# Kernel tuning notes

Hardware: AMD Instinct MI355X
Metric: run time of the kernel (lower is better)

The kernel has to match this reference:

```python
import jax, jax.numpy as jnp
import numpy as np

N, E = 50000, 800000
IN_DIM, OUT_DIM, HEADS, ORDER = 128, 32, 4, 2
HID = OUT_DIM * HEADS  # 128
NEG_SLOPE = 0.2
LN_EPS = 1e-5


def setup_inputs() -> dict:
    key = jax.random.key(0)
    ks = jax.random.split(key, 16)
    inp = {
        'features': jax.random.normal(ks[0], (N, IN_DIM), jnp.float32),
        'src': jax.random.randint(ks[1], (E,), 0, N, jnp.int32),
        'dst': jax.random.randint(ks[2], (E,), 0, N, jnp.int32),
    }
    in_dims = [IN_DIM, HID]
    for i in range(ORDER):
        d_in = in_dims[i]
        s = 1.0 / np.sqrt(d_in)
        inp[f'W{i}'] = jax.random.normal(ks[3 + 5 * i], (d_in, HID), jnp.float32) * s
        inp[f'al{i}'] = jax.random.normal(ks[4 + 5 * i], (HEADS, OUT_DIM), jnp.float32) * 0.1
        inp[f'ar{i}'] = jax.random.normal(ks[5 + 5 * i], (HEADS, OUT_DIM), jnp.float32) * 0.1
        inp[f'b{i}'] = jnp.zeros((HID,), jnp.float32)
        inp[f'g{i}'] = jnp.ones((HID,), jnp.float32)
        inp[f'be{i}'] = jnp.zeros((HID,), jnp.float32)
    return inp


def _gat_layer(x, src, dst, W, al, ar, b):
    # x: [N, d_in] -> h: [N, H, D]
    h = (x @ W).reshape(N, HEADS, OUT_DIM)
    el = jnp.sum(h * al, axis=-1)  # [N, H]
    er = jnp.sum(h * ar, axis=-1)  # [N, H]
    e = jax.nn.leaky_relu(el[src] + er[dst], NEG_SLOPE)  # [E, H]
    # segment softmax over incoming edges of each dst node
    m = jax.ops.segment_max(e, dst, num_segments=N)  # [N, H]
    ex = jnp.exp(e - m[dst])  # [E, H]
    denom = jax.ops.segment_sum(ex, dst, num_segments=N)  # [N, H]
    alpha = ex / jnp.maximum(denom[dst], 1e-9)  # [E, H]
    msg = h[src] * alpha[:, :, None]  # [E, H, D]
    out = jax.ops.segment_sum(msg, dst, num_segments=N)  # [N, H, D]
    return out.reshape(N, HID) + b


def _layernorm(x, g, be):
    mu = jnp.mean(x, axis=-1, keepdims=True)
    var = jnp.mean(jnp.square(x - mu), axis=-1, keepdims=True)
    return (x - mu) * jax.lax.rsqrt(var + LN_EPS) * g + be


def reference(features, src, dst, W0, al0, ar0, b0, g0, be0, W1, al1, ar1, b1, g1, be1):
    feats = features
    params = [(W0, al0, ar0, b0, g0, be0), (W1, al1, ar1, b1, g1, be1)]
    for (W, al, ar, b, g, be) in params:
        feats = _gat_layer(feats, src, dst, W, al, ar, b)
        feats = _layernorm(feats, g, be)
        feats = jax.nn.elu(feats)
    return feats
```

## Files before the change

kernel.cpp:

```cpp
#include <hip/hip_runtime.h>
#include <hip/hip_bf16.h>

#define N_NODES 50000
#define E_EDGES 800000
#define HID 128
#define HEADS 4
#define NEG_SLOPE 0.2f
#define LN_EPS 1e-5f
#define PARAM_FLOATS 17024
#define NBUCK 196
#define BCAP 6144
#define BIN_CH 2048
#define CVT_BLOCKS 67

typedef __attribute__((ext_vector_type(8))) short short8;
typedef __attribute__((ext_vector_type(4))) float float4v;
typedef __fp16 hf2 __attribute__((ext_vector_type(2)));

__device__ __forceinline__ float bf2f(__hip_bfloat16 b) { return __bfloat162float(b); }
__device__ __forceinline__ short bfb(float f) {
    __hip_bfloat16 h = __float2bfloat16(f);
    return *(short*)&h;
}
__device__ __forceinline__ float leaky(float v) { return v > 0.f ? v : v * NEG_SLOPE; }

__device__ __forceinline__ unsigned int f2ord(float f) {
    unsigned int u = __float_as_uint(f);
    return (u & 0x80000000u) ? ~u : (u | 0x80000000u);
}
__device__ __forceinline__ float ord2f(unsigned int u) {
    u = (u & 0x80000000u) ? (u & 0x7FFFFFFFu) : ~u;
    return __uint_as_float(u);
}

__device__ __forceinline__ unsigned int pair_lo(unsigned int a, unsigned int b) {
#if __has_builtin(__builtin_amdgcn_perm)
    return __builtin_amdgcn_perm(b, a, 0x05040100);
#else
    return (a & 0xFFFFu) | (b << 16);
#endif
}
__device__ __forceinline__ unsigned int pair_hi(unsigned int a, unsigned int b) {
#if __has_builtin(__builtin_amdgcn_perm)
    return __builtin_amdgcn_perm(b, a, 0x07060302);
#else
    return (a >> 16) | (b & 0xFFFF0000u);
#endif
}
__device__ __forceinline__ float dot2acc(unsigned int hpair, unsigned int epair, float acc) {
#if __has_builtin(__builtin_amdgcn_fdot2)
    return __builtin_amdgcn_fdot2(__builtin_bit_cast(hf2, hpair),
                                  __builtin_bit_cast(hf2, epair), acc, false);
#else
    hf2 hv = __builtin_bit_cast(hf2, hpair);
    hf2 ev = __builtin_bit_cast(hf2, epair);
    return fmaf((float)hv.x, (float)ev.x, fmaf((float)hv.y, (float)ev.y, acc));
#endif
}
__device__ __forceinline__ unsigned int pk_f16x2(float a, float b) {
#if __has_builtin(__builtin_amdgcn_cvt_pkrtz)
    auto r = __builtin_amdgcn_cvt_pkrtz(a, b);
    return __builtin_bit_cast(unsigned int, r);
#else
    hf2 r = { (__fp16)a, (__fp16)b };
    return __builtin_bit_cast(unsigned int, r);
#endif
}

__global__ __launch_bounds__(256) void cvt_params_kernel(
    const void* W0, const void* al0, const void* ar0, const void* b0,
    const void* g0, const void* be0,
    const void* W1, const void* al1, const void* ar1, const void* b1,
    const void* g1, const void* be1,
    float* __restrict__ out0, float* __restrict__ out1,
    unsigned short* __restrict__ wt0, unsigned short* __restrict__ wt1,
    unsigned int* __restrict__ flag, unsigned int* __restrict__ gmax0,
    unsigned int* __restrict__ gmax1, int* __restrict__ bcnt) {
    int t = threadIdx.x;
    const unsigned int* w0p = (const unsigned int*)W0;
    int cnt = 0;
    for (int i = t; i < 4096; i += 256) {
        unsigned int lo = (w0p[i] & 0xFFFFu) << 16;
        float v = fabsf(__uint_as_float(lo));
        if (v >= 1e-6f && v <= 1.0f) cnt++;
    }
#pragma unroll
    for (int off = 32; off >= 1; off >>= 1) cnt += __shfl_xor(cnt, off);
    __shared__ int shm[4];
    if ((t & 63) == 0) shm[t >> 6] = cnt;
    __syncthreads();
    unsigned int isb = ((shm[0] + shm[1] + shm[2] + shm[3]) > 2048) ? 1u : 0u;

    if (blockIdx.x == 0) {
        if (t == 0) *flag = isb;
        if (t < 4) {
            gmax0[t] = f2ord(-INFINITY);
            gmax1[t] = f2ord(-INFINITY);
        }
        if (t < NBUCK) bcnt[t] = 0;
    }

    int blk = blockIdx.x;
    int layer = 0;
    if (blk >= CVT_BLOCKS) { layer = 1; blk -= CVT_BLOCKS; }
    int i = blk * 256 + t;
    if (i >= PARAM_FLOATS) return;

    const void *W, *al, *ar, *b, *g, *be;
    float* out;
    unsigned short* wt;
    if (layer == 0) {
        W = W0; al = al0; ar = ar0; b = b0; g = g0; be = be0;
        out = out0; wt = wt0;
    } else {
        W = W1; al = al1; ar = ar1; b = b1; g = g1; be = be1;
        out = out1; wt = wt1;
    }

    if (i < 16384) {
        unsigned short bits;
        if (isb) bits = ((const unsigned short*)W)[i];
        else     { short s = bfb(((const float*)W)[i]); bits = (unsigned short)s; }
        wt[((i & 127) << 7) | (i >> 7)] = bits;
        return;
    }
    const void* src; int off;
    if (i < 16512)      { src = al; off = i - 16384; }
    else if (i < 16640) { src = ar; off = i - 16512; }
    else if (i < 16768) { src = b;  off = i - 16640; }
    else if (i < 16896) { src = g;  off = i - 16768; }
    else                { src = be; off = i - 16896; }
    out[i] = isb ? bf2f(((const __hip_bfloat16*)src)[off]) : ((const float*)src)[off];
}

__global__ __launch_bounds__(256) void bin_kernel(const int* __restrict__ src,
                                                  const int* __restrict__ dst,
                                                  int* __restrict__ bcnt,
                                                  unsigned int* __restrict__ ebuf) {
    __shared__ int lh[NBUCK];
    __shared__ int lbase[NBUCK];
    int t = threadIdx.x;
    for (int i = t; i < NBUCK; i += 256) lh[i] = 0;
    __syncthreads();
    int e0 = blockIdx.x * BIN_CH;
    int n = min(BIN_CH, E_EDGES - e0);
    int s8[8], d8[8], rk[8];
#pragma unroll
    for (int j = 0; j < 8; ++j) {
        int k = j * 256 + t;
        if (k < n) {
            s8[j] = src[e0 + k];
            d8[j] = dst[e0 + k];
            rk[j] = atomicAdd(&lh[d8[j] >> 8], 1);
        }
    }
    __syncthreads();
    for (int i = t; i < NBUCK; i += 256) lbase[i] = atomicAdd(&bcnt[i], lh[i]);
    __syncthreads();
#pragma unroll
    for (int j = 0; j < 8; ++j) {
        int k = j * 256 + t;
        if (k < n) {
            int b = d8[j] >> 8;
            int pos = lbase[b] + rk[j];
            if (pos < BCAP)
                ebuf[b * BCAP + pos] = ((unsigned int)s8[j] << 8) | (unsigned int)(d8[j] & 255);
        }
    }
}

__global__ __launch_bounds__(256) void csr_kernel(const int* __restrict__ bcnt,
                                                  const unsigned int* __restrict__ ebuf,
                                                  int* __restrict__ offs,
                                                  int* __restrict__ esrc) {
    __shared__ int cnt[256];
    __shared__ int wt[4];
    __shared__ int sbase[256];
    __shared__ int out_lds[BCAP];
    int b = blockIdx.x, t = threadIdx.x;
    int lane = t & 63, wid = t >> 6;

    int bv = (t < NBUCK) ? min(bcnt[t], BCAP) : 0;
    {
        int x = bv;
#pragma unroll
        for (int o = 1; o < 64; o <<= 1) {
            int y = __shfl_up(x, o);
            if (lane >= o) x += y;
        }
        if (lane == 63) wt[wid] = x;
        __syncthreads();
        int add = 0;
        for (int j = 0; j < wid; j++) add += wt[j];
        sbase[t] = add + x - bv;
    }
    __syncthreads();
    int base = sbase[b];
    int n = min(bcnt[b], BCAP);
    const unsigned int* eb = ebuf + b * BCAP;
    cnt[t] = 0;
    __syncthreads();
    for (int i = t; i < n; i += 256) atomicAdd(&cnt[eb[i] & 255u], 1);
    __syncthreads();
    int v = cnt[t];
    int x = v;
#pragma unroll
    for (int o = 1; o < 64; o <<= 1) {
        int y = __shfl_up(x, o);
        if (lane >= o) x += y;
    }
    if (lane == 63) wt[wid] = x;
    __syncthreads();
    int add = 0;
    for (int j = 0; j < wid; j++) add += wt[j];
    int excl = add + x - v;
    int node = b * 256 + t;
    if (node <= N_NODES) offs[node] = base + excl;
    __syncthreads();
    cnt[t] = excl;
    __syncthreads();
    for (int i = t; i < n; i += 256) {
        unsigned int e = eb[i];
        int p = atomicAdd(&cnt[e & 255u], 1);
        out_lds[p] = (int)(e >> 8);
    }
    __syncthreads();
    for (int i = t; i < n; i += 256) esrc[base + i] = out_lds[i];
}

__global__ __launch_bounds__(256) void gemm_mfma_kernel(const void* __restrict__ xin,
                                                        const unsigned short* __restrict__ wt,
                                                        const float* __restrict__ params,
                                                        const unsigned int* __restrict__ flag,
                                                        int mode,
                                                        unsigned int* __restrict__ hh,
                                                        float* __restrict__ el,
                                                        float* __restrict__ er,
                                                        unsigned int* __restrict__ gmax,
                                                        int M) {
    __shared__ float ldsC[4][16][132];
    __shared__ unsigned int smax[4];
    unsigned int isb = mode ? 1u : *flag;
    int t = threadIdx.x;
    if (t < 4) smax[t] = 0u;
    int w = t >> 6, lane = t & 63;
    int m = lane & 15, quad = lane >> 4;
    int row0b = blockIdx.x * 64;
    int arow = row0b + w * 16 + m;
    bool avalid = arow < M;

    float4v acc[8];
#pragma unroll
    for (int i = 0; i < 8; i++) acc[i] = (float4v){0.f, 0.f, 0.f, 0.f};

#pragma unroll
    for (int kt = 0; kt < 4; ++kt) {
        short8 a = (short8){0, 0, 0, 0, 0, 0, 0, 0};
        if (avalid) {
            int base = arow * 128 + kt * 32 + quad * 8;
            if (isb) {
                a = *(const short8*)((const unsigned short*)xin + base);
            } else {
                const float* xp = (const float*)xin + base;
                float4 f0 = *(const float4*)xp;
                float4 f1 = *(const float4*)(xp + 4);
                a = (short8){bfb(f0.x), bfb(f0.y), bfb(f0.z), bfb(f0.w),
                             bfb(f1.x), bfb(f1.y), bfb(f1.z), bfb(f1.w)};
            }
        }
#pragma unroll
        for (int ct = 0; ct < 8; ++ct) {
            short8 b = *(const short8*)(wt + (ct * 16 + m) * 128 + kt * 32 + quad * 8);
            acc[ct] = __builtin_amdgcn_mfma_f32_16x16x32_bf16(a, b, acc[ct], 0, 0, 0);
        }
    }

#pragma unroll
    for (int ct = 0; ct < 8; ++ct)
#pragma unroll
        for (int r = 0; r < 4; ++r)
            ldsC[w][quad * 4 + r][ct * 16 + m] = acc[ct][r];
    __syncthreads();

    int c0 = (t & 15) * 8;
    int r0e = (t >> 4) * 4;
    float al8[8], ar8[8];
#pragma unroll
    for (int j = 0; j < 8; j++) {
        al8[j] = params[16384 + c0 + j];
        ar8[j] = params[16512 + c0 + j];
    }
    int head = (lane & 15) >> 2;
    float elmax = -INFINITY;

#pragma unroll
    for (int i = 0; i < 4; i++) {
        int rr = r0e + i;
        int row = row0b + rr;
        bool ok = row < M;
        const float* ld = &ldsC[rr >> 4][rr & 15][c0];
        float4 h0 = *(const float4*)ld;
        float4 h1 = *(const float4*)(ld + 4);
        float hv[8] = {h0.x, h0.y, h0.z, h0.w, h1.x, h1.y, h1.z, h1.w};
        if (ok) {
            unsigned int u0 = pk_f16x2(hv[0], hv[1]);
            unsigned int u1 = pk_f16x2(hv[2], hv[3]);
            unsigned int u2 = pk_f16x2(hv[4], hv[5]);
            unsigned int u3 = pk_f16x2(hv[6], hv[7]);
            *(uint4*)(hh + row * 64 + (c0 >> 1)) = make_uint4(u0, u1, u2, u3);
        }
        float e_l = 0.f, e_r = 0.f;
#pragma unroll
        for (int j = 0; j < 8; j++) {
            e_l = fmaf(hv[j], al8[j], e_l);
            e_r = fmaf(hv[j], ar8[j], e_r);
        }
        e_l += __shfl_xor(e_l, 1); e_l += __shfl_xor(e_l, 2);
        e_r += __shfl_xor(e_r, 1); e_r += __shfl_xor(e_r, 2);
        if (ok && (lane & 3) == 0) {
            el[row * 4 + head] = e_l;
            er[row * 4 + head] = e_r;
            elmax = fmaxf(elmax, e_l);
        }
    }
    elmax = fmaxf(elmax, __shfl_xor(elmax, 16));
    elmax = fmaxf(elmax, __shfl_xor(elmax, 32));
    __syncthreads();
    if ((lane & 15) == 0 || (lane & 15) == 4 || (lane & 15) == 8 || (lane & 15) == 12) {
        if (elmax > -INFINITY) atomicMax(&smax[head], f2ord(elmax));
    }
    __syncthreads();
    if (t < 4) atomicMax(&gmax[t], smax[t]);
}

template <bool LAST>
__global__ __launch_bounds__(256) void agg_ln_kernel(const int* __restrict__ offs,
                                                     const int* __restrict__ esrc,
                                                     const float* __restrict__ el,
                                                     const float* __restrict__ er,
                                                     const unsigned int* __restrict__ hh,
                                                     const float* __restrict__ params,
                                                     const unsigned int* __restrict__ gmax,
                                                     const unsigned int* __restrict__ flag,
                                                     unsigned int* __restrict__ x_next,
                                                     void* __restrict__ out) {
    int node = (blockIdx.x * 256 + threadIdx.x) >> 6;
    int lane = threadIdx.x & 63;
    if (node >= N_NODES) return;
    int e0 = offs[node], e1 = offs[node + 1];
    int d = e1 - e0;
    int sh = lane & 3;
    int slot = lane >> 2;
    int q = lane >> 4;
    int l4 = lane & 15;
    int hd = l4 >> 2;
    float er_s = er[node * 4 + sh];
    float M = leaky(ord2f(gmax[sh]) + er_s);

    float lsum = 0.f;
    float a0 = 0.f, a1 = 0.f, a2 = 0.f, a3 = 0.f;
    float a4 = 0.f, a5 = 0.f, a6 = 0.f, a7 = 0.f;
    for (int b0 = 0; b0 < d; b0 += 16) {
        int idx = b0 + slot;
        float ex = 0.f;
        int s = 0;
        if (idx < d) {
            s = esrc[e0 + idx];
            ex = __expf(leaky(el[s * 4 + sh] + er_s) - M);
        }
        lsum += ex;
        __fp16 e16 = (__fp16)ex;
        unsigned int pk = ((unsigned int)s << 16)
                        | (unsigned int)__builtin_bit_cast(unsigned short, e16);
#pragma unroll
        for (int jp = 0; jp < 2; ++jp) {
            unsigned int q1 = __shfl(pk, (jp * 8 + q) * 4 + hd);
            unsigned int q2 = __shfl(pk, (jp * 8 + 4 + q) * 4 + hd);
            int s1 = (int)(q1 >> 16);
            int s2 = (int)(q2 >> 16);
            uint4 p = *(const uint4*)(hh + s1 * 64 + l4 * 4);
            uint4 r = *(const uint4*)(hh + s2 * 64 + l4 * 4);
            unsigned int e2 = pair_lo(q1, q2);
            a0 = dot2acc(pair_lo(p.x, r.x), e2, a0);
            a1 = dot2acc(pair_hi(p.x, r.x), e2, a1);
            a2 = dot2acc(pair_lo(p.y, r.y), e2, a2);
            a3 = dot2acc(pair_hi(p.y, r.y), e2, a3);
            a4 = dot2acc(pair_lo(p.z, r.z), e2, a4);
            a5 = dot2acc(pair_hi(p.z, r.z), e2, a5);
            a6 = dot2acc(pair_lo(p.w, r.w), e2, a6);
            a7 = dot2acc(pair_hi(p.w, r.w), e2, a7);
        }
    }
#pragma unroll
    for (int off = 4; off <= 32; off <<= 1) lsum += __shfl_xor(lsum, off);
    float l = __shfl(lsum, hd);
    a0 += __shfl_xor(a0, 16); a0 += __shfl_xor(a0, 32);
    a1 += __shfl_xor(a1, 16); a1 += __shfl_xor(a1, 32);
    a2 += __shfl_xor(a2, 16); a2 += __shfl_xor(a2, 32);
    a3 += __shfl_xor(a3, 16); a3 += __shfl_xor(a3, 32);
    a4 += __shfl_xor(a4, 16); a4 += __shfl_xor(a4, 32);
    a5 += __shfl_xor(a5, 16); a5 += __shfl_xor(a5, 32);
    a6 += __shfl_xor(a6, 16); a6 += __shfl_xor(a6, 32);
    a7 += __shfl_xor(a7, 16); a7 += __shfl_xor(a7, 32);

    float inv = 1.f / fmaxf(l, 1e-9f);
    int c0 = l4 * 8;
    float4 ba = *(const float4*)(params + 16640 + c0);
    float4 bb = *(const float4*)(params + 16640 + c0 + 4);
    float v0 = fmaf(a0, inv, ba.x);
    float v1 = fmaf(a1, inv, ba.y);
    float v2 = fmaf(a2, inv, ba.z);
    float v3 = fmaf(a3, inv, ba.w);
    float v4 = fmaf(a4, inv, bb.x);
    float v5 = fmaf(a5, inv, bb.y);
    float v6 = fmaf(a6, inv, bb.z);
    float v7 = fmaf(a7, inv, bb.w);

    float s1 = (v0 + v1) + (v2 + v3) + (v4 + v5) + (v6 + v7);
    float s2 = (v0 * v0 + v1 * v1) + (v2 * v2 + v3 * v3)
             + (v4 * v4 + v5 * v5) + (v6 * v6 + v7 * v7);
#pragma unroll
    for (int off = 1; off <= 8; off <<= 1) {
        s1 += __shfl_xor(s1, off);
        s2 += __shfl_xor(s2, off);
    }
    float mu = s1 * (1.f / 128.f);
    float var = fmaxf(s2 * (1.f / 128.f) - mu * mu, 0.f);
    float rstd = rsqrtf(var + LN_EPS);
    float4 ga = *(const float4*)(params + 16768 + c0);
    float4 gb = *(const float4*)(params + 16768 + c0 + 4);
    float4 ea = *(const float4*)(params + 16896 + c0);
    float4 eb = *(const float4*)(params + 16896 + c0 + 4);
    float y0 = (v0 - mu) * rstd * ga.x + ea.x;
    float y1 = (v1 - mu) * rstd * ga.y + ea.y;
    float y2 = (v2 - mu) * rstd * ga.z + ea.z;
    float y3 = (v3 - mu) * rstd * ga.w + ea.w;
    float y4 = (v4 - mu) * rstd * gb.x + eb.x;
    float y5 = (v5 - mu) * rstd * gb.y + eb.y;
    float y6 = (v6 - mu) * rstd * gb.z + eb.z;
    float y7 = (v7 - mu) * rstd * gb.w + eb.w;
    y0 = y0 > 0.f ? y0 : (__expf(y0) - 1.f);
    y1 = y1 > 0.f ? y1 : (__expf(y1) - 1.f);
    y2 = y2 > 0.f ? y2 : (__expf(y2) - 1.f);
    y3 = y3 > 0.f ? y3 : (__expf(y3) - 1.f);
    y4 = y4 > 0.f ? y4 : (__expf(y4) - 1.f);
    y5 = y5 > 0.f ? y5 : (__expf(y5) - 1.f);
    y6 = y6 > 0.f ? y6 : (__expf(y6) - 1.f);
    y7 = y7 > 0.f ? y7 : (__expf(y7) - 1.f);

    if (q == 0) {
        if (LAST && !*flag) {
            *(float4*)((float*)out + node * 128 + c0) = make_float4(y0, y1, y2, y3);
            *(float4*)((float*)out + node * 128 + c0 + 4) = make_float4(y4, y5, y6, y7);
        } else {
            uint4 pk4;
            pk4.x = (unsigned int)(unsigned short)bfb(y0)
                  | ((unsigned int)(unsigned short)bfb(y1) << 16);
            pk4.y = (unsigned int)(unsigned short)bfb(y2)
                  | ((unsigned int)(unsigned short)bfb(y3) << 16);
            pk4.z = (unsigned int)(unsigned short)bfb(y4)
                  | ((unsigned int)(unsigned short)bfb(y5) << 16);
            pk4.w = (unsigned int)(unsigned short)bfb(y6)
                  | ((unsigned int)(unsigned short)bfb(y7) << 16);
            unsigned int* dst = LAST ? (unsigned int*)out : x_next;
            *(uint4*)(dst + node * 64 + l4 * 4) = pk4;
        }
    }
}

extern "C" void kernel_launch(void* const* d_in, const int* in_sizes, int n_in,
                              void* d_out, int out_size, void* d_ws, size_t ws_size,
                              hipStream_t stream) {
    const void* features = d_in[0];
    const int* src = (const int*)d_in[1];
    const int* dst = (const int*)d_in[2];

    char* w = (char*)d_ws;
    unsigned int* xbuf = (unsigned int*)w;
    unsigned int* hh = (unsigned int*)(w + 12800000);
    float* el = (float*)(w + 25600000);
    float* er = (float*)(w + 26400000);
    float* params0 = (float*)(w + 27200000);
    float* params1 = params0 + PARAM_FLOATS;
    unsigned short* wt0 = (unsigned short*)(w + 27337000);
    unsigned short* wt1 = wt0 + 16384;
    int* offs = (int*)(w + 27403000);
    int* esrc = (int*)(w + 27604000);
    int* bcnt  = (int*)(w + 30804992);
    unsigned int* flag  = (unsigned int*)(w + 30806848);
    unsigned int* gmax0 = (unsigned int*)(w + 30806912);
    unsigned int* gmax1 = (unsigned int*)(w + 30806976);
    unsigned int* ebuf = (unsigned int*)(w + 30807040);

    cvt_params_kernel<<<2 * CVT_BLOCKS, 256, 0, stream>>>(
        d_in[3], d_in[4], d_in[5], d_in[6], d_in[7], d_in[8],
        d_in[9], d_in[10], d_in[11], d_in[12], d_in[13], d_in[14],
        params0, params1, wt0, wt1, flag, gmax0, gmax1, bcnt);

    bin_kernel<<<(E_EDGES + BIN_CH - 1) / BIN_CH, 256, 0, stream>>>(src, dst, bcnt, ebuf);
    csr_kernel<<<NBUCK, 256, 0, stream>>>(bcnt, ebuf, offs, esrc);

    for (int l = 0; l < 2; ++l) {
        float* params = (l == 0) ? params0 : params1;
        unsigned short* wt = (l == 0) ? wt0 : wt1;
        unsigned int* gmax = (l == 0) ? gmax0 : gmax1;
        const void* x = (l == 0) ? features : (const void*)xbuf;
        int mode = (l == 0) ? 0 : 1;

        gemm_mfma_kernel<<<(N_NODES + 63) / 64, 256, 0, stream>>>(
            x, wt, params, flag, mode, hh, el, er, gmax, N_NODES);
        if (l == 0) {
            agg_ln_kernel<false><<<(N_NODES * 64 + 255) / 256, 256, 0, stream>>>(
                offs, esrc, el, er, hh, params, gmax, flag, xbuf, nullptr);
        } else {
            agg_ln_kernel<true><<<(N_NODES * 64 + 255) / 256, 256, 0, stream>>>(
                offs, esrc, el, er, hh, params, gmax, flag, nullptr, d_out);
        }
    }
}
```

Before: 259.3 us.

## Precompute per-edge exp weights in separate kernel, simplify aggregation loop

Adds an edge-parallel kernel that computes the four per-head softmax numerators for every CSR edge and packs them with the source index into a 16-byte record. The aggregation kernel then reads these records directly instead of gathering el/er, computing exp, and shuffling packed values between lanes. The per-head denominator is accumulated with a dot2 against ones. The CSR stage now also stores the destination node alongside the source. This removes the shuffles and the redundant exp work from the latency-bound gather loop, at the cost of an extra launch per layer and about 12.8 MB of extra writes and reads per layer. The denominator is now summed from fp16-rounded values.

```diff
diff --git a/kernel.cpp b/kernel.cpp
--- a/kernel.cpp
+++ b/kernel.cpp
@@ -33,6 +33,14 @@
     return __uint_as_float(u);
 }
 
+__device__ __forceinline__ unsigned int pair_sel(unsigned int a, unsigned int b,
+                                                 unsigned int pmask, int hi) {
+#if __has_builtin(__builtin_amdgcn_perm)
+    return __builtin_amdgcn_perm(b, a, pmask);
+#else
+    return hi ? ((a >> 16) | (b & 0xFFFF0000u)) : ((a & 0xFFFFu) | (b << 16));
+#endif
+}
 __device__ __forceinline__ unsigned int pair_lo(unsigned int a, unsigned int b) {
 #if __has_builtin(__builtin_amdgcn_perm)
     return __builtin_amdgcn_perm(b, a, 0x05040100);
@@ -172,7 +180,7 @@
 __global__ __launch_bounds__(256) void csr_kernel(const int* __restrict__ bcnt,
                                                   const unsigned int* __restrict__ ebuf,
                                                   int* __restrict__ offs,
-                                                  int* __restrict__ esrc) {
+                                                  unsigned int* __restrict__ edat) {
     __shared__ int cnt[256];
     __shared__ int wt[4];
     __shared__ int sbase[256];
@@ -222,10 +230,13 @@
     for (int i = t; i < n; i += 256) {
         unsigned int e = eb[i];
         int p = atomicAdd(&cnt[e & 255u], 1);
-        out_lds[p] = (int)(e >> 8);
-    }
-    __syncthreads();
-    for (int i = t; i < n; i += 256) esrc[base + i] = out_lds[i];
+        out_lds[p] = (int)e;
+    }
+    __syncthreads();
+    for (int i = t; i < n; i += 256) {
+        unsigned int e = (unsigned int)out_lds[i];
+        edat[base + i] = ((e >> 8) << 16) | ((unsigned int)(b * 256) + (e & 255u));
+    }
 }
 
 __global__ __launch_bounds__(256) void gemm_mfma_kernel(const void* __restrict__ xin,
@@ -333,14 +344,38 @@
     if (t < 4) atomicMax(&gmax[t], smax[t]);
 }
 
+__global__ __launch_bounds__(256) void edge_ex_kernel(const unsigned int* __restrict__ edat,
+                                                      const float* __restrict__ el,
+                                                      const float* __restrict__ er,
+                                                      const unsigned int* __restrict__ gmax,
+                                                      uint4* __restrict__ exb) {
+    int p = blockIdx.x * 256 + threadIdx.x;
+    if (p >= E_EDGES) {
+        if (p < E_EDGES + 16) exb[p] = make_uint4(0, 0, 0, 0);
+        return;
+    }
+    unsigned int u = edat[p];
+    int s = (int)(u >> 16);
+    int dn = (int)(u & 0xFFFFu);
+    float4 elv = *(const float4*)(el + s * 4);
+    float4 erv = *(const float4*)(er + dn * 4);
+    float elvv[4] = {elv.x, elv.y, elv.z, elv.w};
+    float ervv[4] = {erv.x, erv.y, erv.z, erv.w};
+    float ex[4];
+#pragma unroll
+    for (int h = 0; h < 4; ++h) {
+        float M = leaky(ord2f(gmax[h]) + ervv[h]);
+        float e = leaky(elvv[h] + ervv[h]);
+        ex[h] = __expf(e - M);
+    }
+    exb[p] = make_uint4((unsigned int)s, pk_f16x2(ex[0], ex[1]), pk_f16x2(ex[2], ex[3]), 0u);
+}
+
 template <bool LAST>
 __global__ __launch_bounds__(256) void agg_ln_kernel(const int* __restrict__ offs,
-                                                     const int* __restrict__ esrc,
-                                                     const float* __restrict__ el,
-                                                     const float* __restrict__ er,
+                                                     const uint4* __restrict__ exb,
                                                      const unsigned int* __restrict__ hh,
                                                      const float* __restrict__ params,
-                                                     const unsigned int* __restrict__ gmax,
                                                      const unsigned int* __restrict__ flag,
                                                      unsigned int* __restrict__ x_next,
                                                      void* __restrict__ out) {
@@ -349,51 +384,42 @@
     if (node >= N_NODES) return;
     int e0 = offs[node], e1 = offs[node + 1];
     int d = e1 - e0;
-    int sh = lane & 3;
-    int slot = lane >> 2;
     int q = lane >> 4;
     int l4 = lane & 15;
     int hd = l4 >> 2;
-    float er_s = er[node * 4 + sh];
-    float M = leaky(ord2f(gmax[sh]) + er_s);
+    unsigned int pmask = (hd & 1) ? 0x07060302u : 0x05040100u;
+    int wsel_hi = (hd & 2) >> 1;
+    const unsigned int ONEPAIR = 0x3C003C00u;
+    const uint4* exbp = exb + e0;
 
     float lsum = 0.f;
     float a0 = 0.f, a1 = 0.f, a2 = 0.f, a3 = 0.f;
     float a4 = 0.f, a5 = 0.f, a6 = 0.f, a7 = 0.f;
     for (int b0 = 0; b0 < d; b0 += 16) {
-        int idx = b0 + slot;
-        float ex = 0.f;
-        int s = 0;
-        if (idx < d) {
-            s = esrc[e0 + idx];
-            ex = __expf(leaky(el[s * 4 + sh] + er_s) - M);
-        }
-        lsum += ex;
-        __fp16 e16 = (__fp16)ex;
-        unsigned int pk = ((unsigned int)s << 16)
-                        | (unsigned int)__builtin_bit_cast(unsigned short, e16);
 #pragma unroll
         for (int jp = 0; jp < 2; ++jp) {
-            unsigned int q1 = __shfl(pk, (jp * 8 + q) * 4 + hd);
-            unsigned int q2 = __shfl(pk, (jp * 8 + 4 + q) * 4 + hd);
-            int s1 = (int)(q1 >> 16);
-            int s2 = (int)(q2 >> 16);
-            uint4 p = *(const uint4*)(hh + s1 * 64 + l4 * 4);
-            uint4 r = *(const uint4*)(hh + s2 * 64 + l4 * 4);
-            unsigned int e2 = pair_lo(q1, q2);
-            a0 = dot2acc(pair_lo(p.x, r.x), e2, a0);
-            a1 = dot2acc(pair_hi(p.x, r.x), e2, a1);
-            a2 = dot2acc(pair_lo(p.y, r.y), e2, a2);
-            a3 = dot2acc(pair_hi(p.y, r.y), e2, a3);
-            a4 = dot2acc(pair_lo(p.z, r.z), e2, a4);
-            a5 = dot2acc(pair_hi(p.z, r.z), e2, a5);
-            a6 = dot2acc(pair_lo(p.w, r.w), e2, a6);
-            a7 = dot2acc(pair_hi(p.w, r.w), e2, a7);
-        }
-    }
-#pragma unroll
-    for (int off = 4; off <= 32; off <<= 1) lsum += __shfl_xor(lsum, off);
-    float l = __shfl(lsum, hd);
+            int ia = b0 + jp * 8 + q;
+            int ib = ia + 4;
+            uint4 eqA = (ia < d) ? exbp[ia] : make_uint4(0, 0, 0, 0);
+            uint4 eqB = (ib < d) ? exbp[ib] : make_uint4(0, 0, 0, 0);
+            int sA = (int)eqA.x, sB = (int)eqB.x;
+            unsigned int wA = wsel_hi ? eqA.z : eqA.y;
+            unsigned int wB = wsel_hi ? eqB.z : eqB.y;
+            unsigned int epair = pair_sel(wA, wB, pmask, hd & 1);
+            uint4 p = *(const uint4*)(hh + sA * 64 + l4 * 4);
+            uint4 r = *(const uint4*)(hh + sB * 64 + l4 * 4);
+            lsum = dot2acc(epair, ONEPAIR, lsum);
+            a0 = dot2acc(pair_lo(p.x, r.x), epair, a0);
+            a1 = dot2acc(pair_hi(p.x, r.x), epair, a1);
+            a2 = dot2acc(pair_lo(p.y, r.y), epair, a2);
+            a3 = dot2acc(pair_hi(p.y, r.y), epair, a3);
+            a4 = dot2acc(pair_lo(p.z, r.z), epair, a4);
+            a5 = dot2acc(pair_hi(p.z, r.z), epair, a5);
+            a6 = dot2acc(pair_lo(p.w, r.w), epair, a6);
+            a7 = dot2acc(pair_hi(p.w, r.w), epair, a7);
+        }
+    }
+    lsum += __shfl_xor(lsum, 16); lsum += __shfl_xor(lsum, 32);
     a0 += __shfl_xor(a0, 16); a0 += __shfl_xor(a0, 32);
     a1 += __shfl_xor(a1, 16); a1 += __shfl_xor(a1, 32);
     a2 += __shfl_xor(a2, 16); a2 += __shfl_xor(a2, 32);
@@ -403,7 +429,7 @@
     a6 += __shfl_xor(a6, 16); a6 += __shfl_xor(a6, 32);
     a7 += __shfl_xor(a7, 16); a7 += __shfl_xor(a7, 32);
 
-    float inv = 1.f / fmaxf(l, 1e-9f);
+    float inv = 1.f / fmaxf(lsum, 1e-9f);
     int c0 = l4 * 8;
     float4 ba = *(const float4*)(params + 16640 + c0);
     float4 bb = *(const float4*)(params + 16640 + c0 + 4);
@@ -485,12 +511,13 @@
     unsigned short* wt0 = (unsigned short*)(w + 27337000);
     unsigned short* wt1 = wt0 + 16384;
     int* offs = (int*)(w + 27403000);
-    int* esrc = (int*)(w + 27604000);
+    unsigned int* edat = (unsigned int*)(w + 27604000);
     int* bcnt  = (int*)(w + 30804992);
     unsigned int* flag  = (unsigned int*)(w + 30806848);
     unsigned int* gmax0 = (unsigned int*)(w + 30806912);
     unsigned int* gmax1 = (unsigned int*)(w + 30806976);
     unsigned int* ebuf = (unsigned int*)(w + 30807040);
+    uint4* exb = (uint4*)(w + 35700000);
 
     cvt_params_kernel<<<2 * CVT_BLOCKS, 256, 0, stream>>>(
         d_in[3], d_in[4], d_in[5], d_in[6], d_in[7], d_in[8],
@@ -498,7 +525,7 @@
         params0, params1, wt0, wt1, flag, gmax0, gmax1, bcnt);
 
     bin_kernel<<<(E_EDGES + BIN_CH - 1) / BIN_CH, 256, 0, stream>>>(src, dst, bcnt, ebuf);
-    csr_kernel<<<NBUCK, 256, 0, stream>>>(bcnt, ebuf, offs, esrc);
+    csr_kernel<<<NBUCK, 256, 0, stream>>>(bcnt, ebuf, offs, edat);
 
     for (int l = 0; l < 2; ++l) {
         float* params = (l == 0) ? params0 : params1;
@@ -509,12 +536,14 @@
 
         gemm_mfma_kernel<<<(N_NODES + 63) / 64, 256, 0, stream>>>(
             x, wt, params, flag, mode, hh, el, er, gmax, N_NODES);
+        edge_ex_kernel<<<(E_EDGES + 16 + 255) / 256, 256, 0, stream>>>(
+            edat, el, er, gmax, exb);
         if (l == 0) {
             agg_ln_kernel<false><<<(N_NODES * 64 + 255) / 256, 256, 0, stream>>>(
-                offs, esrc, el, er, hh, params, gmax, flag, xbuf, nullptr);
+                offs, exb, hh, params, flag, xbuf, nullptr);
         } else {
             agg_ln_kernel<true><<<(N_NODES * 64 + 255) / 256, 256, 0, stream>>>(
-                offs, esrc, el, er, hh, params, gmax, flag, nullptr, d_out);
-        }
-    }
-}
+                offs, exb, hh, params, flag, nullptr, d_out);
+        }
+    }
+}
```

Measured after the change: 271.8 us. 4.8% more time.
